# Kernel tuning notes

Hardware: AMD Instinct MI355X
Metric: run time of the kernel (lower is better)

The kernel has to match this reference:

```python
import jax, jax.numpy as jnp
import numpy as np

N = 100000   # nodes
E = 1600000  # message edges (avg degree 16)
L = 500000   # supervision (label) edges
IN = 128     # input feature dim
H = 2        # attention heads
C = 64       # hidden_dim per head
HC = H * C   # 128, per-layer output channels
DEC = 64     # decoder_dim
NEG_SLOPE = 0.2


def setup_inputs():
    key = jax.random.key(0)
    ks = jax.random.split(key, 16)
    s = 0.05
    return {
        "x": jax.random.normal(ks[0], (N, IN), jnp.float32),
        "edge_index": jax.random.randint(ks[1], (2, E), 0, N, dtype=jnp.int64),
        "edge_label_index": jax.random.randint(ks[2], (2, L), 0, N, dtype=jnp.int64),
        "W1": jax.random.normal(ks[3], (IN, HC), jnp.float32) * s,
        "att_src1": jax.random.normal(ks[4], (H, C), jnp.float32) * s,
        "att_dst1": jax.random.normal(ks[5], (H, C), jnp.float32) * s,
        "bias1": jnp.zeros((HC,), jnp.float32),
        "W2": jax.random.normal(ks[6], (HC, HC), jnp.float32) * s,
        "att_src2": jax.random.normal(ks[7], (H, C), jnp.float32) * s,
        "att_dst2": jax.random.normal(ks[8], (H, C), jnp.float32) * s,
        "bias2": jnp.zeros((HC,), jnp.float32),
        "lin1_w": jax.random.normal(ks[9], (2 * HC, DEC), jnp.float32) * s,
        "lin1_b": jnp.zeros((DEC,), jnp.float32),
        "lin2_w": jax.random.normal(ks[10], (DEC, 1), jnp.float32) * s,
        "lin2_b": jnp.zeros((1,), jnp.float32),
    }


def _gat_conv(x, src, dst, W, att_src, att_dst, bias, n_nodes):
    # PyG GATConv (concat=True, negative_slope=0.2), self-loops already in src/dst.
    h = (x @ W).reshape(-1, H, C)                       # [N, H, C]
    a_s = jnp.sum(h * att_src[None], axis=-1)           # [N, H]
    a_d = jnp.sum(h * att_dst[None], axis=-1)           # [N, H]
    e = jax.nn.leaky_relu(a_s[src] + a_d[dst], NEG_SLOPE)  # [E, H]
    m = jax.ops.segment_max(e, dst, num_segments=n_nodes)  # segment-softmax (stable)
    ex = jnp.exp(e - jax.lax.stop_gradient(m)[dst])
    denom = jax.ops.segment_sum(ex, dst, num_segments=n_nodes)
    alpha = ex / denom[dst]                             # [E, H]
    out = jax.ops.segment_sum(h[src] * alpha[:, :, None], dst, num_segments=n_nodes)
    return out.reshape(n_nodes, HC) + bias


def reference(x, edge_index, edge_label_index, W1, att_src1, att_dst1, bias1,
              W2, att_src2, att_dst2, bias2, lin1_w, lin1_b, lin2_w, lin2_b):
    n = x.shape[0]
    loop = jnp.arange(n, dtype=edge_index.dtype)
    src = jnp.concatenate([edge_index[0], loop])
    dst = jnp.concatenate([edge_index[1], loop])
    # encode (eval mode: dropout is a no-op)
    h1 = jax.nn.relu(_gat_conv(x, src, dst, W1, att_src1, att_dst1, bias1, n))
    z = _gat_conv(h1, src, dst, W2, att_src2, att_dst2, bias2, n)
    # decode
    hs = jnp.concatenate([z[edge_label_index[0]], z[edge_label_index[1]]], axis=1)
    hdec = jax.nn.relu(hs @ lin1_w + lin1_b)
    return (hdec @ lin2_w + lin2_b).reshape(-1)
```

## Files before the change

kernel.cpp:

```cpp
#include <hip/hip_runtime.h>
#include <hip/hip_fp16.h>


typedef _Float16 f16x8 __attribute__((ext_vector_type(8)));
typedef float f32x4 __attribute__((ext_vector_type(4)));

__device__ __forceinline__ float rl_f(float v, int lane) {
    return __int_as_float(__builtin_amdgcn_readlane(__float_as_int(v), lane));
}

__device__ __forceinline__ void fma_mix_lo(float& acc, unsigned hv, float e) {
    asm("v_fma_mix_f32 %0, %1, %2, %0 op_sel_hi:[1,0,0]"
        : "+v"(acc) : "v"(hv), "v"(e));
}
__device__ __forceinline__ void fma_mix_hi(float& acc, unsigned hv, float e) {
    asm("v_fma_mix_f32 %0, %1, %2, %0 op_sel:[1,0,0] op_sel_hi:[1,0,0]"
        : "+v"(acc) : "v"(hv), "v"(e));
}

#define WT_LD 136
__global__ __launch_bounds__(256, 3) void gemm_mfma(
    const float* __restrict__ X, const float* __restrict__ W,
    _Float16* __restrict__ Y, int nrows,
    const float* __restrict__ att_s, const float* __restrict__ att_d,
    float2* __restrict__ as_out, float2* __restrict__ ad_out)
{
    __shared__ _Float16 WT[128 * WT_LD];
    __shared__ _Float16 At[64 * WT_LD];
    const int t = threadIdx.x;
    const int lane = t & 63;
    const int wid = t >> 6;

    for (int i = t; i < 128 * 32; i += 256) {
        const int k = i >> 5;
        const int n4 = (i & 31) * 4;
        const float4 wv = *reinterpret_cast<const float4*>(&W[k * 128 + n4]);
        WT[(n4 + 0) * WT_LD + k] = (_Float16)wv.x;
        WT[(n4 + 1) * WT_LD + k] = (_Float16)wv.y;
        WT[(n4 + 2) * WT_LD + k] = (_Float16)wv.z;
        WT[(n4 + 3) * WT_LD + k] = (_Float16)wv.w;
    }

    const int am = lane & 15, ag = lane >> 4;
    const int pr = t >> 2;
    const int pc = (t & 3) * 32;

    float asv[8], adv[8];
    if (as_out) {
#pragma unroll
        for (int n0 = 0; n0 < 8; ++n0) {
            asv[n0] = att_s[n0 * 16 + am];
            adv[n0] = att_d[n0 * 16 + am];
        }
    }

    float4 pf[8];
    auto load_pf = [&](int tbase) {
        const int gr = tbase + pr;
        if (gr < nrows) {
            const float* src = X + (size_t)gr * 128 + pc;
#pragma unroll
            for (int q = 0; q < 8; ++q)
                pf[q] = *reinterpret_cast<const float4*>(src + q * 4);
        } else {
#pragma unroll
            for (int q = 0; q < 8; ++q) pf[q] = make_float4(0.f, 0.f, 0.f, 0.f);
        }
    };
    auto write_pf = [&]() {
        _Float16 tmp[32];
#pragma unroll
        for (int q = 0; q < 8; ++q) {
            tmp[q * 4 + 0] = (_Float16)pf[q].x; tmp[q * 4 + 1] = (_Float16)pf[q].y;
            tmp[q * 4 + 2] = (_Float16)pf[q].z; tmp[q * 4 + 3] = (_Float16)pf[q].w;
        }
#pragma unroll
        for (int q = 0; q < 4; ++q)
            *reinterpret_cast<f16x8*>(&At[pr * WT_LD + pc + q * 8]) =
                *reinterpret_cast<const f16x8*>(&tmp[q * 8]);
    };

    const int ntiles = (nrows + 63) >> 6;
    int tile = blockIdx.x;
    if (tile < ntiles) load_pf(tile * 64);

    for (; tile < ntiles; tile += gridDim.x) {
        const int rbase = tile * 64;
        __syncthreads();
        write_pf();
        __syncthreads();

        const int nt = tile + gridDim.x;
        if (nt < ntiles) load_pf(nt * 64);

        const int srow = wid * 16;
        f16x8 a[4];
#pragma unroll
        for (int kb = 0; kb < 4; ++kb)
            a[kb] = *reinterpret_cast<const f16x8*>(
                &At[(srow + am) * WT_LD + kb * 32 + ag * 8]);

        f32x4 acc[8];
#pragma unroll
        for (int n0 = 0; n0 < 8; ++n0) {
            f32x4 c = {0.f, 0.f, 0.f, 0.f};
#pragma unroll
            for (int kb = 0; kb < 4; ++kb) {
                const f16x8 b = *reinterpret_cast<const f16x8*>(
                    &WT[(n0 * 16 + am) * WT_LD + kb * 32 + ag * 8]);
                c = __builtin_amdgcn_mfma_f32_16x16x32_f16(a[kb], b, c, 0, 0, 0);
            }
            acc[n0] = c;
        }

        const int growbase = rbase + srow + ag * 4;

#pragma unroll
        for (int j = 0; j < 4; ++j) {
            const int grow = growbase + j;
            if (grow < nrows) {
#pragma unroll
                for (int n0 = 0; n0 < 8; ++n0)
                    Y[(size_t)grow * 128 + n0 * 16 + am] = (_Float16)acc[n0][j];
            }
        }

        if (as_out) {
#pragma unroll
            for (int j = 0; j < 4; ++j) {
                float s0 = 0.f, s1 = 0.f, d0 = 0.f, d1 = 0.f;
#pragma unroll
                for (int n0 = 0; n0 < 4; ++n0) {
                    s0 = fmaf(acc[n0][j], asv[n0], s0);
                    d0 = fmaf(acc[n0][j], adv[n0], d0);
                }
#pragma unroll
                for (int n0 = 4; n0 < 8; ++n0) {
                    s1 = fmaf(acc[n0][j], asv[n0], s1);
                    d1 = fmaf(acc[n0][j], adv[n0], d1);
                }
#pragma unroll
                for (int off = 1; off < 16; off <<= 1) {
                    s0 += __shfl_xor(s0, off, 64); s1 += __shfl_xor(s1, off, 64);
                    d0 += __shfl_xor(d0, off, 64); d1 += __shfl_xor(d1, off, 64);
                }
                const int grow = growbase + j;
                if (am == 0 && grow < nrows) {
                    as_out[grow] = make_float2(s0, s1);
                    ad_out[grow] = make_float2(d0, d1);
                }
            }
        }
    }
}

__global__ __launch_bounds__(256) void hist_xcd_k(
    const int* __restrict__ edst, int E, int* __restrict__ counts, int npp)
{
    const int part = blockIdx.x & 7;
    const int lo = part * npp;
    const int hiN = lo + npp;
    const int bi = blockIdx.x >> 3;
    const int stride = (gridDim.x >> 3) * blockDim.x;
    for (int e = bi * blockDim.x + threadIdx.x; e < E; e += stride) {
        const int d = edst[e];
        if (d >= lo && d < hiN) atomicAdd(&counts[d], 1);
    }
}

__global__ __launch_bounds__(256) void scan_phase1(
    const int* __restrict__ counts, int* __restrict__ blockSums, int N)
{
    __shared__ int wsum[4];
    const int b = blockIdx.x, t = threadIdx.x;
    const int base = b * 1024 + t * 4;
    int s = 0;
    if (base + 3 < N) {
        const int4 c = *reinterpret_cast<const int4*>(&counts[base]);
        s = c.x + c.y + c.z + c.w + 4;
    } else {
#pragma unroll
        for (int k = 0; k < 4; ++k) if (base + k < N) s += counts[base + k] + 1;
    }
#pragma unroll
    for (int off = 32; off; off >>= 1) s += __shfl_xor(s, off, 64);
    if ((t & 63) == 0) wsum[t >> 6] = s;
    __syncthreads();
    if (t == 0) blockSums[b] = wsum[0] + wsum[1] + wsum[2] + wsum[3];
}

__global__ __launch_bounds__(256) void scan_phase2(
    int* __restrict__ blockSums, int nb, int* __restrict__ row_ptr, int N)
{
    __shared__ int wsum[4];
    __shared__ int carry_sh;
    const int t = threadIdx.x;
    if (t == 0) carry_sh = 0;
    __syncthreads();
    for (int base = 0; base < nb; base += 256) {
        const int i = base + t;
        const int v = (i < nb) ? blockSums[i] : 0;
        int x = v;
#pragma unroll
        for (int off = 1; off < 64; off <<= 1) {
            const int y = __shfl_up(x, off, 64);
            if ((t & 63) >= off) x += y;
        }
        if ((t & 63) == 63) wsum[t >> 6] = x;
        __syncthreads();
        int woff = 0;
        for (int w = 0; w < (t >> 6); ++w) woff += wsum[w];
        const int carry = carry_sh;
        if (i < nb) blockSums[i] = carry + woff + x - v;
        __syncthreads();
        if (t == 255) carry_sh = carry + woff + x;
        __syncthreads();
    }
    if (t == 0) row_ptr[N] = carry_sh;
}

__global__ __launch_bounds__(256) void scan_phase3(
    const int* __restrict__ counts, const int* __restrict__ blockSums,
    int* __restrict__ row_ptr, int* __restrict__ cursor,
    int* __restrict__ csr_src, int N)
{
    __shared__ int wsum[4];
    const int b = blockIdx.x, t = threadIdx.x;
    const int base = b * 1024 + t * 4;
    int v0 = 0, v1 = 0, v2 = 0, v3 = 0;
    if (base + 3 < N) {
        const int4 c = *reinterpret_cast<const int4*>(&counts[base]);
        v0 = c.x + 1; v1 = c.y + 1; v2 = c.z + 1; v3 = c.w + 1;
    } else {
        if (base + 0 < N) v0 = counts[base + 0] + 1;
        if (base + 1 < N) v1 = counts[base + 1] + 1;
        if (base + 2 < N) v2 = counts[base + 2] + 1;
        if (base + 3 < N) v3 = counts[base + 3] + 1;
    }
    const int tsum = v0 + v1 + v2 + v3;
    int x = tsum;
#pragma unroll
    for (int off = 1; off < 64; off <<= 1) {
        const int y = __shfl_up(x, off, 64);
        if ((t & 63) >= off) x += y;
    }
    if ((t & 63) == 63) wsum[t >> 6] = x;
    __syncthreads();
    int woff = 0;
    for (int w = 0; w < (t >> 6); ++w) woff += wsum[w];
    int excl = blockSums[b] + woff + x - tsum;
    int p = excl;
    if (base + 0 < N) { row_ptr[base + 0] = p; csr_src[p] = base + 0; cursor[base + 0] = p + 1; p += v0; }
    if (base + 1 < N) { row_ptr[base + 1] = p; csr_src[p] = base + 1; cursor[base + 1] = p + 1; p += v1; }
    if (base + 2 < N) { row_ptr[base + 2] = p; csr_src[p] = base + 2; cursor[base + 2] = p + 1; p += v2; }
    if (base + 3 < N) { row_ptr[base + 3] = p; csr_src[p] = base + 3; cursor[base + 3] = p + 1; }
}

__global__ __launch_bounds__(256) void scatter_xcd_k(
    const int* __restrict__ esrc, const int* __restrict__ edst, int E,
    int* __restrict__ cursor, int* __restrict__ csr_src, int npp)
{
    const int part = blockIdx.x & 7;
    const int lo = part * npp;
    const int hiN = lo + npp;
    const int bi = blockIdx.x >> 3;
    const int stride = (gridDim.x >> 3) * blockDim.x;
    for (int e = bi * blockDim.x + threadIdx.x; e < E; e += stride) {
        const int d = edst[e];
        if (d >= lo && d < hiN) {
            const int pos = atomicAdd(&cursor[d], 1);
            csr_src[pos] = esrc[e];
        }
    }
}

__global__ __launch_bounds__(256) void csr_aggregate(
    const int* __restrict__ row_ptr, const int* __restrict__ csr_src,
    const unsigned* __restrict__ h2u, const float2* __restrict__ as_,
    const float2* __restrict__ ad_, const float* __restrict__ bias,
    float* __restrict__ out, int N, int do_relu)
{
    const int lane = threadIdx.x & 63;
    const int node = (blockIdx.x * blockDim.x + threadIdx.x) >> 6;
    if (node >= N) return;
    const int l32 = lane & 31;
    const int half = lane >> 5;
    const bool head1 = l32 >= 16;

    const int start = row_ptr[node];
    const int end   = row_ptr[node + 1];
    const float2 ad = ad_[node];

    float den0 = 0.f, den1 = 0.f;
    float acc0 = 0.f, acc1 = 0.f, acc2 = 0.f, acc3 = 0.f;

    for (int base = start; base < end; base += 64) {
        const int cnt = min(64, end - base);
        float ex0 = 0.f, ex1 = 0.f;
        int s = 0;
        if (lane < cnt) {
            s = csr_src[base + lane];
            const float2 as = as_[s];
            float e0 = as.x + ad.x; e0 = fmaxf(e0, 0.2f * e0);
            float e1 = as.y + ad.y; e1 = fmaxf(e1, 0.2f * e1);
            ex0 = __expf(e0); ex1 = __expf(e1);
            den0 += ex0; den1 += ex1;
        }
        int j = 0;
        for (; j + 8 <= cnt; j += 8) {
            uint2 hv[4]; float e[4];
#pragma unroll
            for (int q = 0; q < 4; ++q) {
                const int jA = j + 2 * q, jB = jA + 1;
                const int sA = __builtin_amdgcn_readlane(s, jA);
                const int sB = __builtin_amdgcn_readlane(s, jB);
                const float eA = head1 ? rl_f(ex1, jA) : rl_f(ex0, jA);
                const float eB = head1 ? rl_f(ex1, jB) : rl_f(ex0, jB);
                e[q] = half ? eB : eA;
                const int src = half ? sB : sA;
                hv[q] = *reinterpret_cast<const uint2*>(
                    h2u + (unsigned)(src * 64 + l32 * 2));
            }
#pragma unroll
            for (int q = 0; q < 4; ++q) {
                fma_mix_lo(acc0, hv[q].x, e[q]);
                fma_mix_hi(acc1, hv[q].x, e[q]);
                fma_mix_lo(acc2, hv[q].y, e[q]);
                fma_mix_hi(acc3, hv[q].y, e[q]);
            }
        }
        for (; j < cnt; j += 2) {
            const int jA = j, jB = j + 1;
            const int sA = __builtin_amdgcn_readlane(s, jA);
            const int sB = __builtin_amdgcn_readlane(s, jB);
            const float eA = head1 ? rl_f(ex1, jA) : rl_f(ex0, jA);
            const float eB = head1 ? rl_f(ex1, jB) : rl_f(ex0, jB);
            const float e = half ? eB : eA;
            const int src = half ? sB : sA;
            const uint2 hv = *reinterpret_cast<const uint2*>(
                h2u + (unsigned)(src * 64 + l32 * 2));
            fma_mix_lo(acc0, hv.x, e);
            fma_mix_hi(acc1, hv.x, e);
            fma_mix_lo(acc2, hv.y, e);
            fma_mix_hi(acc3, hv.y, e);
        }
    }

    acc0 += __shfl_xor(acc0, 32, 64);
    acc1 += __shfl_xor(acc1, 32, 64);
    acc2 += __shfl_xor(acc2, 32, 64);
    acc3 += __shfl_xor(acc3, 32, 64);

#pragma unroll
    for (int off = 32; off; off >>= 1) {
        den0 += __shfl_xor(den0, off, 64);
        den1 += __shfl_xor(den1, off, 64);
    }

    if (half == 0) {
        const float rd = 1.f / (head1 ? den1 : den0);
        const float4 bv = *reinterpret_cast<const float4*>(&bias[l32 * 4]);
        float4 v;
        v.x = fmaf(acc0, rd, bv.x);
        v.y = fmaf(acc1, rd, bv.y);
        v.z = fmaf(acc2, rd, bv.z);
        v.w = fmaf(acc3, rd, bv.w);
        if (do_relu) {
            v.x = fmaxf(v.x, 0.f); v.y = fmaxf(v.y, 0.f);
            v.z = fmaxf(v.z, 0.f); v.w = fmaxf(v.w, 0.f);
        }
        *reinterpret_cast<float4*>(&out[(size_t)node * 128 + l32 * 4]) = v;
    }
}

__global__ void build_wuv(const float* __restrict__ lin1_w, float* __restrict__ Wuv)
{
    const int i = blockIdx.x * blockDim.x + threadIdx.x;
    if (i >= 128 * 128) return;
    const int k = i >> 7, j = i & 127;
    Wuv[i] = (j < 64) ? lin1_w[k * 64 + j] : lin1_w[(128 + k) * 64 + (j - 64)];
}

__global__ __launch_bounds__(256) void decode_k(
    const int* __restrict__ eli, int L_, const unsigned* __restrict__ uvd,
    const float* __restrict__ lin1_b, const float* __restrict__ lin2_w,
    const float* __restrict__ lin2_b, float* __restrict__ out)
{
    const int lane = threadIdx.x & 63;
    const int l32 = lane & 31;
    const int half = lane >> 5;
    const int pstride = (gridDim.x * blockDim.x) >> 6;
    const float2 bv = ((const float2*)lin1_b)[l32];
    const float2 wv = ((const float2*)lin2_w)[l32];
    const float b2 = lin2_b[0];
    const int npairs = (L_ + 1) >> 1;
    for (int pid = (blockIdx.x * blockDim.x + threadIdx.x) >> 6; pid < npairs; pid += pstride) {
        const int w = min(pid * 2 + half, L_ - 1);
        const int a = eli[w], b = eli[L_ + w];
        const unsigned ua = uvd[(unsigned)(a * 64 + l32)];
        const unsigned vb = uvd[(unsigned)(b * 64 + 32 + l32)];
        float x0 = bv.x, x1 = bv.y;
        asm("v_fma_mix_f32 %0, %1, 1.0, %0 op_sel_hi:[1,0,0]" : "+v"(x0) : "v"(ua));
        asm("v_fma_mix_f32 %0, %1, 1.0, %0 op_sel:[1,0,0] op_sel_hi:[1,0,0]" : "+v"(x1) : "v"(ua));
        asm("v_fma_mix_f32 %0, %1, 1.0, %0 op_sel_hi:[1,0,0]" : "+v"(x0) : "v"(vb));
        asm("v_fma_mix_f32 %0, %1, 1.0, %0 op_sel:[1,0,0] op_sel_hi:[1,0,0]" : "+v"(x1) : "v"(vb));
        x0 = fmaxf(x0, 0.f); x1 = fmaxf(x1, 0.f);
        float p = fmaf(x0, wv.x, x1 * wv.y);
#pragma unroll
        for (int off = 1; off < 32; off <<= 1) p += __shfl_xor(p, off, 64);
        if (l32 == 0 && pid * 2 + half < L_) out[pid * 2 + half] = p + b2;
    }
}

extern "C" void kernel_launch(void* const* d_in, const int* in_sizes, int n_in,
                              void* d_out, int out_size, void* d_ws, size_t ws_size,
                              hipStream_t stream)
{
    const float* x     = (const float*)d_in[0];
    const int*   ei    = (const int*)d_in[1];
    const int*   eli   = (const int*)d_in[2];
    const float* W1    = (const float*)d_in[3];
    const float* atts1 = (const float*)d_in[4];
    const float* attd1 = (const float*)d_in[5];
    const float* bias1 = (const float*)d_in[6];
    const float* W2    = (const float*)d_in[7];
    const float* atts2 = (const float*)d_in[8];
    const float* attd2 = (const float*)d_in[9];
    const float* bias2 = (const float*)d_in[10];
    const float* lin1w = (const float*)d_in[11];
    const float* lin1b = (const float*)d_in[12];
    const float* lin2w = (const float*)d_in[13];
    const float* lin2b = (const float*)d_in[14];
    float* out = (float*)d_out;

    const int N = in_sizes[0] / 128;
    const int E = in_sizes[1] / 2;
    const int L = in_sizes[2] / 2;

    float* ws   = (float*)d_ws;
    __half2* h16 = (__half2*)ws;
    float* x2z  = ws + (size_t)N * 64;
    float* a_s  = x2z + (size_t)N * 128;
    float* a_d  = a_s + (size_t)N * 2;
    float* Wuv  = a_d + (size_t)N * 2;
    int* row_ptr = (int*)(Wuv + 128 * 128);
    int* counts  = row_ptr + (N + 4);
    int* cursor  = counts + N;
    int* csr_src = cursor + N;
    int* blockSums = csr_src + (E + N);

    const int nb = (N + 1023) / 1024;
    const int npp = (N + 7) / 8;
    const int ntiles = (N + 63) / 64;
    const int gemmGrid = ntiles < 768 ? ntiles : 768;

    hipMemsetAsync(counts, 0, (size_t)N * sizeof(int), stream);
    hist_xcd_k<<<2048, 256, 0, stream>>>(ei + E, E, counts, npp);
    scan_phase1<<<nb, 256, 0, stream>>>(counts, blockSums, N);
    scan_phase2<<<1, 256, 0, stream>>>(blockSums, nb, row_ptr, N);
    scan_phase3<<<nb, 256, 0, stream>>>(counts, blockSums, row_ptr, cursor, csr_src, N);
    scatter_xcd_k<<<2048, 256, 0, stream>>>(ei, ei + E, E, cursor, csr_src, npp);

    for (int layer = 0; layer < 2; ++layer) {
        const float* xin  = (layer == 0) ? x : x2z;
        const float* W    = (layer == 0) ? W1 : W2;
        const float* as_w = (layer == 0) ? atts1 : atts2;
        const float* ad_w = (layer == 0) ? attd1 : attd2;
        const float* bs   = (layer == 0) ? bias1 : bias2;

        gemm_mfma<<<gemmGrid, 256, 0, stream>>>(xin, W, (_Float16*)h16, N, as_w, ad_w,
                                                (float2*)a_s, (float2*)a_d);
        csr_aggregate<<<(N + 3) / 4, 256, 0, stream>>>(row_ptr, csr_src,
                                                       (const unsigned*)h16,
                                                       (const float2*)a_s, (const float2*)a_d,
                                                       bs, x2z, N, (layer == 0) ? 1 : 0);
    }

    build_wuv<<<64, 256, 0, stream>>>(lin1w, Wuv);
    gemm_mfma<<<gemmGrid, 256, 0, stream>>>(x2z, Wuv, (_Float16*)h16, N,
                                            nullptr, nullptr, nullptr, nullptr);
    decode_k<<<8192, 256, 0, stream>>>(eli, L, (const unsigned*)h16,
                                       lin1b, lin2w, lin2b, out);
}
```

Measured before the change: 431.0 us.

## Store layer outputs in fp16 and simplify dst histogram kernel

The aggregation kernel now writes its per-node outputs as fp16 instead of fp32. The following GEMMs (layer 2 and decoder projection) read fp16 directly through a templated load path, which halves the intermediate activation traffic and skips the conversion step. Separately, the XCD-partitioned histogram kernel is replaced by a plain grid-stride atomic histogram, so each edge is read once instead of by every partition. The risks are extra fp16 rounding of hidden activations and more scattered atomic contention in the histogram.

```diff
diff --git a/kernel.cpp b/kernel.cpp
--- a/kernel.cpp
+++ b/kernel.cpp
@@ -19,8 +19,9 @@
 }
 
 #define WT_LD 136
+template<bool FP16IN>
 __global__ __launch_bounds__(256, 3) void gemm_mfma(
-    const float* __restrict__ X, const float* __restrict__ W,
+    const void* __restrict__ Xv, const float* __restrict__ W,
     _Float16* __restrict__ Y, int nrows,
     const float* __restrict__ att_s, const float* __restrict__ att_d,
     float2* __restrict__ as_out, float2* __restrict__ ad_out)
@@ -54,30 +55,49 @@
         }
     }
 
-    float4 pf[8];
+    float4 pff[8];
+    uint4  pfh[4];
     auto load_pf = [&](int tbase) {
         const int gr = tbase + pr;
-        if (gr < nrows) {
-            const float* src = X + (size_t)gr * 128 + pc;
-#pragma unroll
-            for (int q = 0; q < 8; ++q)
-                pf[q] = *reinterpret_cast<const float4*>(src + q * 4);
+        if (FP16IN) {
+            if (gr < nrows) {
+                const uint4* src = reinterpret_cast<const uint4*>(
+                    (const _Float16*)Xv + (size_t)gr * 128 + pc);
+#pragma unroll
+                for (int q = 0; q < 4; ++q) pfh[q] = src[q];
+            } else {
+#pragma unroll
+                for (int q = 0; q < 4; ++q) pfh[q] = make_uint4(0, 0, 0, 0);
+            }
         } else {
-#pragma unroll
-            for (int q = 0; q < 8; ++q) pf[q] = make_float4(0.f, 0.f, 0.f, 0.f);
+            if (gr < nrows) {
+                const float* src = (const float*)Xv + (size_t)gr * 128 + pc;
+#pragma unroll
+                for (int q = 0; q < 8; ++q)
+                    pff[q] = *reinterpret_cast<const float4*>(src + q * 4);
+            } else {
+#pragma unroll
+                for (int q = 0; q < 8; ++q) pff[q] = make_float4(0.f, 0.f, 0.f, 0.f);
+            }
         }
     };
     auto write_pf = [&]() {
-        _Float16 tmp[32];
-#pragma unroll
-        for (int q = 0; q < 8; ++q) {
-            tmp[q * 4 + 0] = (_Float16)pf[q].x; tmp[q * 4 + 1] = (_Float16)pf[q].y;
-            tmp[q * 4 + 2] = (_Float16)pf[q].z; tmp[q * 4 + 3] = (_Float16)pf[q].w;
-        }
-#pragma unroll
-        for (int q = 0; q < 4; ++q)
-            *reinterpret_cast<f16x8*>(&At[pr * WT_LD + pc + q * 8]) =
-                *reinterpret_cast<const f16x8*>(&tmp[q * 8]);
+        if (FP16IN) {
+#pragma unroll
+            for (int q = 0; q < 4; ++q)
+                *reinterpret_cast<uint4*>(&At[pr * WT_LD + pc + q * 8]) = pfh[q];
+        } else {
+            _Float16 tmp[32];
+#pragma unroll
+            for (int q = 0; q < 8; ++q) {
+                tmp[q * 4 + 0] = (_Float16)pff[q].x; tmp[q * 4 + 1] = (_Float16)pff[q].y;
+                tmp[q * 4 + 2] = (_Float16)pff[q].z; tmp[q * 4 + 3] = (_Float16)pff[q].w;
+            }
+#pragma unroll
+            for (int q = 0; q < 4; ++q)
+                *reinterpret_cast<f16x8*>(&At[pr * WT_LD + pc + q * 8]) =
+                    *reinterpret_cast<const f16x8*>(&tmp[q * 8]);
+        }
     };
 
     const int ntiles = (nrows + 63) >> 6;
@@ -154,18 +174,12 @@
     }
 }
 
-__global__ __launch_bounds__(256) void hist_xcd_k(
-    const int* __restrict__ edst, int E, int* __restrict__ counts, int npp)
-{
-    const int part = blockIdx.x & 7;
-    const int lo = part * npp;
-    const int hiN = lo + npp;
-    const int bi = blockIdx.x >> 3;
-    const int stride = (gridDim.x >> 3) * blockDim.x;
-    for (int e = bi * blockDim.x + threadIdx.x; e < E; e += stride) {
-        const int d = edst[e];
-        if (d >= lo && d < hiN) atomicAdd(&counts[d], 1);
-    }
+__global__ __launch_bounds__(256) void hist_k(
+    const int* __restrict__ edst, int E, int* __restrict__ counts)
+{
+    const int stride = gridDim.x * blockDim.x;
+    for (int e = blockIdx.x * blockDim.x + threadIdx.x; e < E; e += stride)
+        atomicAdd(&counts[edst[e]], 1);
 }
 
 __global__ __launch_bounds__(256) void scan_phase1(
@@ -278,7 +292,7 @@
     const int* __restrict__ row_ptr, const int* __restrict__ csr_src,
     const unsigned* __restrict__ h2u, const float2* __restrict__ as_,
     const float2* __restrict__ ad_, const float* __restrict__ bias,
-    float* __restrict__ out, int N, int do_relu)
+    uint2* __restrict__ out16, int N, int do_relu)
 {
     const int lane = threadIdx.x & 63;
     const int node = (blockIdx.x * blockDim.x + threadIdx.x) >> 6;
@@ -360,16 +374,18 @@
     if (half == 0) {
         const float rd = 1.f / (head1 ? den1 : den0);
         const float4 bv = *reinterpret_cast<const float4*>(&bias[l32 * 4]);
-        float4 v;
-        v.x = fmaf(acc0, rd, bv.x);
-        v.y = fmaf(acc1, rd, bv.y);
-        v.z = fmaf(acc2, rd, bv.z);
-        v.w = fmaf(acc3, rd, bv.w);
+        float vx = fmaf(acc0, rd, bv.x);
+        float vy = fmaf(acc1, rd, bv.y);
+        float vz = fmaf(acc2, rd, bv.z);
+        float vw = fmaf(acc3, rd, bv.w);
         if (do_relu) {
-            v.x = fmaxf(v.x, 0.f); v.y = fmaxf(v.y, 0.f);
-            v.z = fmaxf(v.z, 0.f); v.w = fmaxf(v.w, 0.f);
-        }
-        *reinterpret_cast<float4*>(&out[(size_t)node * 128 + l32 * 4]) = v;
+            vx = fmaxf(vx, 0.f); vy = fmaxf(vy, 0.f);
+            vz = fmaxf(vz, 0.f); vw = fmaxf(vw, 0.f);
+        }
+        const __half2 p0 = __float22half2_rn(make_float2(vx, vy));
+        const __half2 p1 = __float22half2_rn(make_float2(vz, vw));
+        out16[(size_t)node * 32 + l32] =
+            make_uint2(*(const unsigned*)&p0, *(const unsigned*)&p1);
     }
 }
 
@@ -438,9 +454,9 @@
     const int L = in_sizes[2] / 2;
 
     float* ws   = (float*)d_ws;
-    __half2* h16 = (__half2*)ws;
-    float* x2z  = ws + (size_t)N * 64;
-    float* a_s  = x2z + (size_t)N * 128;
+    _Float16* h16  = (_Float16*)ws;
+    _Float16* x2z16 = (_Float16*)(ws + (size_t)N * 64);
+    float* a_s  = ws + (size_t)N * 128;
     float* a_d  = a_s + (size_t)N * 2;
     float* Wuv  = a_d + (size_t)N * 2;
     int* row_ptr = (int*)(Wuv + 128 * 128);
@@ -455,30 +471,27 @@
     const int gemmGrid = ntiles < 768 ? ntiles : 768;
 
     hipMemsetAsync(counts, 0, (size_t)N * sizeof(int), stream);
-    hist_xcd_k<<<2048, 256, 0, stream>>>(ei + E, E, counts, npp);
+    hist_k<<<2048, 256, 0, stream>>>(ei + E, E, counts);
     scan_phase1<<<nb, 256, 0, stream>>>(counts, blockSums, N);
     scan_phase2<<<1, 256, 0, stream>>>(blockSums, nb, row_ptr, N);
     scan_phase3<<<nb, 256, 0, stream>>>(counts, blockSums, row_ptr, cursor, csr_src, N);
     scatter_xcd_k<<<2048, 256, 0, stream>>>(ei, ei + E, E, cursor, csr_src, npp);
 
-    for (int layer = 0; layer < 2; ++layer) {
-        const float* xin  = (layer == 0) ? x : x2z;
-        const float* W    = (layer == 0) ? W1 : W2;
-        const float* as_w = (layer == 0) ? atts1 : atts2;
-        const float* ad_w = (layer == 0) ? attd1 : attd2;
-        const float* bs   = (layer == 0) ? bias1 : bias2;
-
-        gemm_mfma<<<gemmGrid, 256, 0, stream>>>(xin, W, (_Float16*)h16, N, as_w, ad_w,
-                                                (float2*)a_s, (float2*)a_d);
-        csr_aggregate<<<(N + 3) / 4, 256, 0, stream>>>(row_ptr, csr_src,
-                                                       (const unsigned*)h16,
-                                                       (const float2*)a_s, (const float2*)a_d,
-                                                       bs, x2z, N, (layer == 0) ? 1 : 0);
-    }
-
+    gemm_mfma<false><<<gemmGrid, 256, 0, stream>>>(x, W1, h16, N, atts1, attd1,
+                                                   (float2*)a_s, (float2*)a_d);
+    csr_aggregate<<<(N + 3) / 4, 256, 0, stream>>>(row_ptr, csr_src,
+                                                   (const unsigned*)h16,
+                                                   (const float2*)a_s, (const float2*)a_d,
+                                                   bias1, (uint2*)x2z16, N, 1);
+    gemm_mfma<true><<<gemmGrid, 256, 0, stream>>>(x2z16, W2, h16, N, atts2, attd2,
+                                                  (float2*)a_s, (float2*)a_d);
+    csr_aggregate<<<(N + 3) / 4, 256, 0, stream>>>(row_ptr, csr_src,
+                                                   (const unsigned*)h16,
+                                                   (const float2*)a_s, (const float2*)a_d,
+                                                   bias2, (uint2*)x2z16, N, 0);
     build_wuv<<<64, 256, 0, stream>>>(lin1w, Wuv);
-    gemm_mfma<<<gemmGrid, 256, 0, stream>>>(x2z, Wuv, (_Float16*)h16, N,
-                                            nullptr, nullptr, nullptr, nullptr);
+    gemm_mfma<true><<<gemmGrid, 256, 0, stream>>>(x2z16, Wuv, h16, N,
+                                                  nullptr, nullptr, nullptr, nullptr);
     decode_k<<<8192, 256, 0, stream>>>(eli, L, (const unsigned*)h16,
                                        lin1b, lin2w, lin2b, out);
 }
```

After: 417.8 us. 1.03x faster.
